# Optimization experiments

Measured on AMD Instinct MI355X. Metric: run time of the kernel, lower is better.

## Reference

```python
import jax, jax.numpy as jnp
import numpy as np

N_NODES = 50000
N_EDGES = 1600000
D_IN = 128
D_HID = 128
D_OUT = 3
EPS = 1e-5


def setup_inputs() -> dict:
    key = jax.random.key(0)
    ks = jax.random.split(key, 16)
    def lin(k, fi, fo):
        s = 1.0 / np.sqrt(fi)
        return jax.random.uniform(k, (fi, fo), jnp.float32, -s, s)
    inp = {
        "x": jax.random.normal(ks[0], (N_NODES, D_IN), jnp.float32),
        "edge_index": jax.random.randint(ks[1], (2, N_EDGES), 0, N_NODES, jnp.int32),
        "W1": lin(ks[2], D_IN, D_HID), "b1": jnp.zeros((D_HID,), jnp.float32),
        "W2": lin(ks[3], D_HID, D_HID), "b2": jnp.zeros((D_HID,), jnp.float32),
        "W3": lin(ks[4], D_HID, D_HID), "b3": jnp.zeros((D_HID,), jnp.float32),
        "g1": jnp.ones((D_HID,), jnp.float32), "beta1": jnp.zeros((D_HID,), jnp.float32),
        "g2": jnp.ones((D_HID,), jnp.float32), "beta2": jnp.zeros((D_HID,), jnp.float32),
        "Wp1": lin(ks[5], D_HID, D_HID), "bp1": jnp.zeros((D_HID,), jnp.float32),
        "Wp2": lin(ks[6], D_HID, D_OUT), "bp2": jnp.zeros((D_OUT,), jnp.float32),
    }
    return inp


def _gcn_norm(edge_index, n):
    # add self-loops, symmetric normalization (PyG GCNConv default)
    loops = jnp.arange(n, dtype=edge_index.dtype)
    row = jnp.concatenate([edge_index[0], loops])  # source
    col = jnp.concatenate([edge_index[1], loops])  # target
    deg = jax.ops.segment_sum(jnp.ones_like(col, jnp.float32), col, num_segments=n)
    dinv = jnp.where(deg > 0, jax.lax.rsqrt(deg), 0.0)
    norm = dinv[row] * dinv[col]  # [E+N]
    return row, col, norm


def _gcn_conv(x, W, b, row, col, norm, n):
    h = x @ W                                # [N, F]
    msg = h[row] * norm[:, None]             # [E+N, F] gather
    out = jax.ops.segment_sum(msg, col, num_segments=n)  # scatter-add
    return out + b


def _layernorm(x, g, beta):
    mu = jnp.mean(x, axis=-1, keepdims=True)
    var = jnp.var(x, axis=-1, keepdims=True)
    return (x - mu) * jax.lax.rsqrt(var + EPS) * g + beta


def reference(x, edge_index, W1, b1, W2, b2, W3, b3, g1, beta1, g2, beta2, Wp1, bp1, Wp2, bp2):
    n = x.shape[0]
    row, col, norm = _gcn_norm(edge_index, n)
    # layer 0
    h = _gcn_conv(x, W1, b1, row, col, norm, n)
    h = _layernorm(jax.nn.relu(h), g1, beta1)  # dropout = identity (eval mode)
    # layer 1
    h = _gcn_conv(h, W2, b2, row, col, norm, n)
    h = _layernorm(jax.nn.relu(h), g2, beta2)
    # layer 2 (no layernorm)
    h = _gcn_conv(h, W3, b3, row, col, norm, n)
    h = jax.nn.relu(h)
    # post-MP MLP head (dropout = identity in eval)
    h = h @ Wp1 + bp1
    return h @ Wp2 + bp2
```

## Files before the change

kernel.cpp:

```cpp
#include <hip/hip_runtime.h>
#include <hip/hip_bf16.h>

#define EPS_LN 1e-5f
#define NB    256
#define SEGCAP 16384

typedef int ivec4 __attribute__((ext_vector_type(4)));
typedef short bf16x8v __attribute__((ext_vector_type(8)));
typedef float f32x4v __attribute__((ext_vector_type(4)));
typedef unsigned short u16x8 __attribute__((ext_vector_type(8)));


__global__ __launch_bounds__(256) void bucket_hist(const int* __restrict__ col,
                                                   int* __restrict__ chunkBH,
                                                   int E, int per, int nbuck) {
    __shared__ int hist[256];
    int t = threadIdx.x;
    hist[t] = 0;
    __syncthreads();
    int s0 = blockIdx.x * per;
    int s1 = s0 + per; if (s1 > E) s1 = E;
    if (s0 < s1) {
        int q0 = s0 >> 2, q1 = s1 >> 2;
        for (int i = q0 + t; i < q1; i += 256) {
            ivec4 c = __builtin_nontemporal_load((const ivec4*)col + i);
            atomicAdd(&hist[c.x >> 8], 1);
            atomicAdd(&hist[c.y >> 8], 1);
            atomicAdd(&hist[c.z >> 8], 1);
            atomicAdd(&hist[c.w >> 8], 1);
        }
        for (int i = (q1 << 2) + t; i < s1; i += 256)
            atomicAdd(&hist[col[i] >> 8], 1);
    }
    __syncthreads();
    if (t < nbuck) chunkBH[blockIdx.x * 256 + t] = hist[t];
}

__global__ __launch_bounds__(256) void bucket_scan(int* __restrict__ chunkBH,
                                                   int* __restrict__ bucketStart,
                                                   int* __restrict__ rowPtr,
                                                   int E, int n, int nbuck, int nb) {
    __shared__ int tot[256];
    int t = threadIdx.x;
    int run = 0;
    if (t < nbuck) {
        for (int k0 = 0; k0 < nb; k0 += 16) {
            int v[16];
#pragma unroll
            for (int j = 0; j < 16; j++)
                v[j] = (k0 + j < nb) ? chunkBH[(k0 + j) * 256 + t] : 0;
#pragma unroll
            for (int j = 0; j < 16; j++) {
                int tv = v[j];
                if (k0 + j < nb) chunkBH[(k0 + j) * 256 + t] = run;
                run += tv;
            }
        }
    }
    tot[t] = run;
    __syncthreads();
    for (int d = 1; d < 256; d <<= 1) {
        int add = (t >= d) ? tot[t - d] : 0;
        __syncthreads();
        tot[t] += add;
        __syncthreads();
    }
    if (t < nbuck) bucketStart[t] = tot[t] - run;
    if (t == 0) { bucketStart[nbuck] = E; rowPtr[n] = E; }
}

__global__ __launch_bounds__(256) void scatter_pairs(const int* __restrict__ row,
                                                     const int* __restrict__ col,
                                                     const int* __restrict__ chunkBH,
                                                     const int* __restrict__ bucketStart,
                                                     unsigned long long* __restrict__ tmp,
                                                     int E, int per, int nbuck) {
    __shared__ int curs[256];
    int t = threadIdx.x;
    int k = blockIdx.x;
    curs[t] = (t < nbuck) ? (chunkBH[k * 256 + t] + bucketStart[t]) : 0;
    __syncthreads();
    int s0 = k * per;
    int s1 = s0 + per; if (s1 > E) s1 = E;
    if (s0 >= s1) return;
    int q0 = s0 >> 2, q1 = s1 >> 2;
    for (int i = q0 + t; i < q1; i += 256) {
        ivec4 c4 = __builtin_nontemporal_load((const ivec4*)col + i);
        ivec4 r4 = __builtin_nontemporal_load((const ivec4*)row + i);
        int p0 = atomicAdd(&curs[c4.x >> 8], 1);
        tmp[p0] = ((unsigned long long)(unsigned)c4.x << 32) | (unsigned)r4.x;
        int p1 = atomicAdd(&curs[c4.y >> 8], 1);
        tmp[p1] = ((unsigned long long)(unsigned)c4.y << 32) | (unsigned)r4.y;
        int p2 = atomicAdd(&curs[c4.z >> 8], 1);
        tmp[p2] = ((unsigned long long)(unsigned)c4.z << 32) | (unsigned)r4.z;
        int p3 = atomicAdd(&curs[c4.w >> 8], 1);
        tmp[p3] = ((unsigned long long)(unsigned)c4.w << 32) | (unsigned)r4.w;
    }
    for (int i = (q1 << 2) + t; i < s1; i += 256) {
        int c = col[i], r = row[i];
        int p = atomicAdd(&curs[c >> 8], 1);
        tmp[p] = ((unsigned long long)(unsigned)c << 32) | (unsigned)r;
    }
}

__global__ __launch_bounds__(256) void bucket_fill(const unsigned long long* __restrict__ tmp,
                                                   const int* __restrict__ bucketStart,
                                                   int* __restrict__ rowPtr,
                                                   float* __restrict__ dinv,
                                                   int* __restrict__ srcList,
                                                   int n) {
    __shared__ int cnt[256];
    __shared__ int cur[256];
    __shared__ int seg[SEGCAP];
    int b = blockIdx.x, t = threadIdx.x;
    int node0 = b << 8;
    int s0 = bucketStart[b], s1 = bucketStart[b + 1];
    int len = s1 - s0;
    cnt[t] = 0;
    __syncthreads();
    for (int i = s0 + t; i < s1; i += 256) {
        int c = (int)(tmp[i] >> 32);
        atomicAdd(&cnt[c - node0], 1);
    }
    __syncthreads();
    int v = cnt[t];
    cur[t] = v;
    __syncthreads();
    for (int d = 1; d < 256; d <<= 1) {
        int add = (t >= d) ? cur[t - d] : 0;
        __syncthreads();
        cur[t] += add;
        __syncthreads();
    }
    int excl = cur[t] - v;
    int node = node0 + t;
    if (node < n) {
        rowPtr[node] = s0 + excl;
        dinv[node] = rsqrtf((float)v + 1.0f);
    }
    cur[t] = excl;
    __syncthreads();
    if (len <= SEGCAP) {
        for (int i = s0 + t; i < s1; i += 256) {
            unsigned long long p = tmp[i];
            int c = (int)(p >> 32);
            int r = (int)(p & 0xffffffffu);
            int pos = atomicAdd(&cur[c - node0], 1);
            seg[pos] = r;
        }
        __syncthreads();
        for (int i = t; i < len; i += 256)
            srcList[s0 + i] = seg[i];
    } else {
        for (int i = s0 + t; i < s1; i += 256) {
            unsigned long long p = tmp[i];
            int c = (int)(p >> 32);
            int r = (int)(p & 0xffffffffu);
            int pos = atomicAdd(&cur[c - node0], 1);
            srcList[s0 + pos] = r;
        }
    }
}

__global__ __launch_bounds__(256) void pack_w_all(const float* __restrict__ W1,
                                                  const float* __restrict__ W2,
                                                  const float* __restrict__ W3,
                                                  unsigned short* __restrict__ Wq,
                                                  const float* __restrict__ Wp1,
                                                  const float* __restrict__ bp1,
                                                  const float* __restrict__ Wp2,
                                                  const float* __restrict__ bp2,
                                                  float* __restrict__ Weff,
                                                  float* __restrict__ beff) {
    if (blockIdx.x == 192) {
        __shared__ float w2[384];
        int t = threadIdx.x;
        for (int idx = t; idx < 384; idx += 256) w2[idx] = Wp2[idx];
        __syncthreads();
        if (t < 128) {
            float p0 = 0.f, p1 = 0.f, p2 = 0.f;
            const float* wr = Wp1 + (size_t)t * 128;
            for (int k = 0; k < 128; k++) {
                float v = wr[k];
                p0 += v * w2[k * 3 + 0];
                p1 += v * w2[k * 3 + 1];
                p2 += v * w2[k * 3 + 2];
            }
            Weff[t * 3 + 0] = p0; Weff[t * 3 + 1] = p1; Weff[t * 3 + 2] = p2;
            if (t == 0) {
                float q0 = bp2[0], q1 = bp2[1], q2 = bp2[2];
                for (int k = 0; k < 128; k++) {
                    float v = bp1[k];
                    q0 += v * w2[k * 3 + 0];
                    q1 += v * w2[k * 3 + 1];
                    q2 += v * w2[k * 3 + 2];
                }
                beff[0] = q0; beff[1] = q1; beff[2] = q2;
            }
        }
        return;
    }
    int w = blockIdx.x >> 6;
    const float* W = (w == 0) ? W1 : (w == 1) ? W2 : W3;
    unsigned short* Wp = Wq + (size_t)w * 32768;
    int s = (blockIdx.x & 63) * 256 + threadIdx.x;
    int i = s & 7;
    int lane = (s >> 3) & 63;
    int jt = (s >> 9) & 7;
    int kb = s >> 12;
    int k = kb * 32 + ((lane >> 4) & 3) * 8 + i;
    int nn = jt * 16 + (lane & 15);
    float v = W[k * 128 + nn];
    __hip_bfloat16 hi = __float2bfloat16(v);
    float hf = __bfloat162float(hi);
    __hip_bfloat16 lo = __float2bfloat16(v - hf);
    Wp[s]         = *(unsigned short*)&hi;
    Wp[16384 + s] = *(unsigned short*)&lo;
}

__device__ __forceinline__ void split8(const float* __restrict__ p,
                                       bf16x8v& ah, bf16x8v& al) {
#pragma unroll
    for (int i = 0; i < 8; i++) {
        float v = p[i];
        __hip_bfloat16 hb = __float2bfloat16(v);
        float hf = __bfloat162float(hb);
        __hip_bfloat16 lb = __float2bfloat16(v - hf);
        ah[i] = *(short*)&hb;
        al[i] = *(short*)&lb;
    }
}

template<int ASRC>
__global__ __launch_bounds__(256) void gemm_mfma(const float* __restrict__ Af32,
                                                 const unsigned short* __restrict__ Ahi,
                                                 const unsigned short* __restrict__ Alo,
                                                 const unsigned short* __restrict__ Wp,
                                                 const float* __restrict__ dinv,
                                                 unsigned short* __restrict__ hbOut,
                                                 int n) {
    __shared__ unsigned short Bs[8192];

    const int tx = threadIdx.x;
    const int wv = tx >> 6;
    const int l  = tx & 63;
    const int m0 = blockIdx.x * 64 + wv * 16;
    int arow = m0 + (l & 15);
    if (arow >= n) arow = 0;
    const int kofs = (l >> 4) * 8;

    f32x4v acc[8];
#pragma unroll
    for (int jt = 0; jt < 8; jt++) acc[jt] = (f32x4v){0.f, 0.f, 0.f, 0.f};

#pragma unroll
    for (int kb = 0; kb < 4; kb++) {
        __syncthreads();
        {
            u16x8* dH = (u16x8*)&Bs[tx * 16];
            const u16x8* sH = (const u16x8*)(Wp + kb * 4096 + tx * 16);
            dH[0] = sH[0]; dH[1] = sH[1];
            u16x8* dL = (u16x8*)&Bs[4096 + tx * 16];
            const u16x8* sL = (const u16x8*)(Wp + 16384 + kb * 4096 + tx * 16);
            dL[0] = sL[0]; dL[1] = sL[1];
        }
        bf16x8v ah, al;
        if (ASRC == 0) {
            split8(Af32 + (size_t)arow * 128 + kb * 32 + kofs, ah, al);
        } else {
            ah = *(const bf16x8v*)(Ahi + (size_t)arow * 128 + kb * 32 + kofs);
            al = *(const bf16x8v*)(Alo + (size_t)arow * 128 + kb * 32 + kofs);
        }
        __syncthreads();
#pragma unroll
        for (int jt = 0; jt < 8; jt++) {
            bf16x8v bh = *(const bf16x8v*)&Bs[jt * 512 + l * 8];
            bf16x8v bl = *(const bf16x8v*)&Bs[4096 + jt * 512 + l * 8];
            acc[jt] = __builtin_amdgcn_mfma_f32_16x16x32_bf16(ah, bh, acc[jt], 0, 0, 0);
            acc[jt] = __builtin_amdgcn_mfma_f32_16x16x32_bf16(ah, bl, acc[jt], 0, 0, 0);
            acc[jt] = __builtin_amdgcn_mfma_f32_16x16x32_bf16(al, bh, acc[jt], 0, 0, 0);
        }
    }

    const int r0 = m0 + (l >> 4) * 4;
    const int colb = l & 15;
#pragma unroll
    for (int r = 0; r < 4; r++) {
        int grow = r0 + r;
        if (grow < n) {
            float dv = dinv[grow];
#pragma unroll
            for (int jt = 0; jt < 8; jt++) {
                __hip_bfloat16 t = __float2bfloat16(acc[jt][r] * dv);
                hbOut[(size_t)grow * 128 + jt * 16 + colb] = *(unsigned short*)&t;
            }
        }
    }
}

#define BF_LO(u) __uint_as_float((u) << 16)
#define BF_HI(u) __uint_as_float((u) & 0xffff0000u)

#define ACC8(u)  do { \
    a[0] += BF_LO((u).x); a[1] += BF_HI((u).x); \
    a[2] += BF_LO((u).y); a[3] += BF_HI((u).y); \
    a[4] += BF_LO((u).z); a[5] += BF_HI((u).z); \
    a[6] += BF_LO((u).w); a[7] += BF_HI((u).w); } while (0)

__global__ __launch_bounds__(128) void agg_post(const unsigned int* __restrict__ hb,
                                                const int* __restrict__ rowPtr,
                                                const int* __restrict__ srcList,
                                                const float* __restrict__ dinv,
                                                const float* __restrict__ b,
                                                const float* __restrict__ g,
                                                const float* __restrict__ beta,
                                                unsigned short* __restrict__ outHi,
                                                unsigned short* __restrict__ outLo,
                                                int n) {
    int wid = (blockIdx.x * 128 + threadIdx.x) >> 6;
    int lane = threadIdx.x & 63;
    if (wid >= n) return;
    int h = lane & 15;
    int gg = lane >> 4;
    int e0 = rowPtr[wid], e1 = rowPtr[wid + 1];
    float dc = dinv[wid];
    const uint4* hb4 = (const uint4*)hb;

    uint4 us = hb4[(size_t)wid * 16 + h];

    float a[8];
#pragma unroll
    for (int j = 0; j < 8; j++) a[j] = 0.f;

    int idx0 = (e0 + 0 + gg < e1) ? srcList[e0 + 0 + gg] : -1;
    int idx1 = (e0 + 4 + gg < e1) ? srcList[e0 + 4 + gg] : -1;
    int idx2 = (e0 + 8 + gg < e1) ? srcList[e0 + 8 + gg] : -1;
    int idx3 = (e0 + 12 + gg < e1) ? srcList[e0 + 12 + gg] : -1;
    int e = e0;
    for (; e + 16 <= e1; e += 16) {
        int ni0 = (e + 16 + gg < e1) ? srcList[e + 16 + gg] : -1;
        int ni1 = (e + 20 + gg < e1) ? srcList[e + 20 + gg] : -1;
        int ni2 = (e + 24 + gg < e1) ? srcList[e + 24 + gg] : -1;
        int ni3 = (e + 28 + gg < e1) ? srcList[e + 28 + gg] : -1;
        uint4 u0 = hb4[(size_t)idx0 * 16 + h];
        uint4 u1 = hb4[(size_t)idx1 * 16 + h];
        uint4 u2 = hb4[(size_t)idx2 * 16 + h];
        uint4 u3 = hb4[(size_t)idx3 * 16 + h];
        ACC8(u0); ACC8(u1); ACC8(u2); ACC8(u3);
        idx0 = ni0; idx1 = ni1; idx2 = ni2; idx3 = ni3;
    }
    if (idx0 >= 0) { uint4 u = hb4[(size_t)idx0 * 16 + h]; ACC8(u); }
    if (idx1 >= 0) { uint4 u = hb4[(size_t)idx1 * 16 + h]; ACC8(u); }
    if (idx2 >= 0) { uint4 u = hb4[(size_t)idx2 * 16 + h]; ACC8(u); }
    if (idx3 >= 0) { uint4 u = hb4[(size_t)idx3 * 16 + h]; ACC8(u); }

#pragma unroll
    for (int j = 0; j < 8; j++) {
        a[j] += __shfl_xor(a[j], 16, 64);
        a[j] += __shfl_xor(a[j], 32, 64);
    }
    ACC8(us);

    float4 bv0 = *(const float4*)(b + h * 8);
    float4 bv1 = *(const float4*)(b + h * 8 + 4);
    a[0] = fmaxf(a[0] * dc + bv0.x, 0.f);
    a[1] = fmaxf(a[1] * dc + bv0.y, 0.f);
    a[2] = fmaxf(a[2] * dc + bv0.z, 0.f);
    a[3] = fmaxf(a[3] * dc + bv0.w, 0.f);
    a[4] = fmaxf(a[4] * dc + bv1.x, 0.f);
    a[5] = fmaxf(a[5] * dc + bv1.y, 0.f);
    a[6] = fmaxf(a[6] * dc + bv1.z, 0.f);
    a[7] = fmaxf(a[7] * dc + bv1.w, 0.f);

    float s = ((a[0] + a[1]) + (a[2] + a[3])) + ((a[4] + a[5]) + (a[6] + a[7]));
#pragma unroll
    for (int m = 8; m >= 1; m >>= 1) s += __shfl_xor(s, m, 64);
    float mu = s * (1.f / 128.f);
    float sq = 0.f;
    float d[8];
#pragma unroll
    for (int j = 0; j < 8; j++) { d[j] = a[j] - mu; sq += d[j] * d[j]; }
#pragma unroll
    for (int m = 8; m >= 1; m >>= 1) sq += __shfl_xor(sq, m, 64);
    float rs = rsqrtf(sq * (1.f / 128.f) + EPS_LN);
    float4 gv0 = *(const float4*)(g + h * 8);
    float4 gv1 = *(const float4*)(g + h * 8 + 4);
    float4 bt0 = *(const float4*)(beta + h * 8);
    float4 bt1 = *(const float4*)(beta + h * 8 + 4);
    a[0] = d[0] * rs * gv0.x + bt0.x;
    a[1] = d[1] * rs * gv0.y + bt0.y;
    a[2] = d[2] * rs * gv0.z + bt0.z;
    a[3] = d[3] * rs * gv0.w + bt0.w;
    a[4] = d[4] * rs * gv1.x + bt1.x;
    a[5] = d[5] * rs * gv1.y + bt1.y;
    a[6] = d[6] * rs * gv1.z + bt1.z;
    a[7] = d[7] * rs * gv1.w + bt1.w;

    if (gg == 0) {
        ushort4 h0, h1, l0, l1;
        __hip_bfloat16 bb; float ff;
        bb = __float2bfloat16(a[0]); ff = __bfloat162float(bb); h0.x = *(unsigned short*)&bb;
        bb = __float2bfloat16(a[0] - ff); l0.x = *(unsigned short*)&bb;
        bb = __float2bfloat16(a[1]); ff = __bfloat162float(bb); h0.y = *(unsigned short*)&bb;
        bb = __float2bfloat16(a[1] - ff); l0.y = *(unsigned short*)&bb;
        bb = __float2bfloat16(a[2]); ff = __bfloat162float(bb); h0.z = *(unsigned short*)&bb;
        bb = __float2bfloat16(a[2] - ff); l0.z = *(unsigned short*)&bb;
        bb = __float2bfloat16(a[3]); ff = __bfloat162float(bb); h0.w = *(unsigned short*)&bb;
        bb = __float2bfloat16(a[3] - ff); l0.w = *(unsigned short*)&bb;
        bb = __float2bfloat16(a[4]); ff = __bfloat162float(bb); h1.x = *(unsigned short*)&bb;
        bb = __float2bfloat16(a[4] - ff); l1.x = *(unsigned short*)&bb;
        bb = __float2bfloat16(a[5]); ff = __bfloat162float(bb); h1.y = *(unsigned short*)&bb;
        bb = __float2bfloat16(a[5] - ff); l1.y = *(unsigned short*)&bb;
        bb = __float2bfloat16(a[6]); ff = __bfloat162float(bb); h1.z = *(unsigned short*)&bb;
        bb = __float2bfloat16(a[6] - ff); l1.z = *(unsigned short*)&bb;
        bb = __float2bfloat16(a[7]); ff = __bfloat162float(bb); h1.w = *(unsigned short*)&bb;
        bb = __float2bfloat16(a[7] - ff); l1.w = *(unsigned short*)&bb;
        size_t base = (size_t)wid * 128 + h * 8;
        *(ushort4*)(outHi + base)     = h0;
        *(ushort4*)(outHi + base + 4) = h1;
        *(ushort4*)(outLo + base)     = l0;
        *(ushort4*)(outLo + base + 4) = l1;
    }
}

__global__ __launch_bounds__(128) void agg_head(
        const unsigned int* __restrict__ hb,
        const int* __restrict__ rowPtr,
        const int* __restrict__ srcList,
        const float* __restrict__ dinv,
        const float* __restrict__ b,
        const float* __restrict__ Weff,
        const float* __restrict__ beff,
        float* __restrict__ out, int n) {
    int tt = threadIdx.x;
    int wid = (blockIdx.x * 128 + tt) >> 6;
    int lane = tt & 63;
    if (wid >= n) return;
    int h = lane & 15;
    int gg = lane >> 4;
    int e0 = rowPtr[wid], e1 = rowPtr[wid + 1];
    float dc = dinv[wid];
    const uint4* hb4 = (const uint4*)hb;
    uint4 us = hb4[(size_t)wid * 16 + h];

    float wreg[24];
    {
        const float4* wp = (const float4*)(Weff + 24 * h);
#pragma unroll
        for (int q = 0; q < 6; q++) {
            float4 v = wp[q];
            wreg[4 * q + 0] = v.x; wreg[4 * q + 1] = v.y;
            wreg[4 * q + 2] = v.z; wreg[4 * q + 3] = v.w;
        }
    }

    float a[8];
#pragma unroll
    for (int j = 0; j < 8; j++) a[j] = 0.f;

    int idx0 = (e0 + 0 + gg < e1) ? srcList[e0 + 0 + gg] : -1;
    int idx1 = (e0 + 4 + gg < e1) ? srcList[e0 + 4 + gg] : -1;
    int idx2 = (e0 + 8 + gg < e1) ? srcList[e0 + 8 + gg] : -1;
    int idx3 = (e0 + 12 + gg < e1) ? srcList[e0 + 12 + gg] : -1;
    int e = e0;
    for (; e + 16 <= e1; e += 16) {
        int ni0 = (e + 16 + gg < e1) ? srcList[e + 16 + gg] : -1;
        int ni1 = (e + 20 + gg < e1) ? srcList[e + 20 + gg] : -1;
        int ni2 = (e + 24 + gg < e1) ? srcList[e + 24 + gg] : -1;
        int ni3 = (e + 28 + gg < e1) ? srcList[e + 28 + gg] : -1;
        uint4 u0 = hb4[(size_t)idx0 * 16 + h];
        uint4 u1 = hb4[(size_t)idx1 * 16 + h];
        uint4 u2 = hb4[(size_t)idx2 * 16 + h];
        uint4 u3 = hb4[(size_t)idx3 * 16 + h];
        ACC8(u0); ACC8(u1); ACC8(u2); ACC8(u3);
        idx0 = ni0; idx1 = ni1; idx2 = ni2; idx3 = ni3;
    }
    if (idx0 >= 0) { uint4 u = hb4[(size_t)idx0 * 16 + h]; ACC8(u); }
    if (idx1 >= 0) { uint4 u = hb4[(size_t)idx1 * 16 + h]; ACC8(u); }
    if (idx2 >= 0) { uint4 u = hb4[(size_t)idx2 * 16 + h]; ACC8(u); }
    if (idx3 >= 0) { uint4 u = hb4[(size_t)idx3 * 16 + h]; ACC8(u); }

#pragma unroll
    for (int j = 0; j < 8; j++) {
        a[j] += __shfl_xor(a[j], 16, 64);
        a[j] += __shfl_xor(a[j], 32, 64);
    }
    ACC8(us);

    float4 bv0 = *(const float4*)(b + h * 8);
    float4 bv1 = *(const float4*)(b + h * 8 + 4);
    a[0] = fmaxf(a[0] * dc + bv0.x, 0.f);
    a[1] = fmaxf(a[1] * dc + bv0.y, 0.f);
    a[2] = fmaxf(a[2] * dc + bv0.z, 0.f);
    a[3] = fmaxf(a[3] * dc + bv0.w, 0.f);
    a[4] = fmaxf(a[4] * dc + bv1.x, 0.f);
    a[5] = fmaxf(a[5] * dc + bv1.y, 0.f);
    a[6] = fmaxf(a[6] * dc + bv1.z, 0.f);
    a[7] = fmaxf(a[7] * dc + bv1.w, 0.f);

    float p0 = 0.f, p1 = 0.f, p2 = 0.f;
#pragma unroll
    for (int j = 0; j < 8; j++) {
        p0 += a[j] * wreg[j * 3 + 0];
        p1 += a[j] * wreg[j * 3 + 1];
        p2 += a[j] * wreg[j * 3 + 2];
    }
#pragma unroll
    for (int m = 8; m >= 1; m >>= 1) {
        p0 += __shfl_xor(p0, m, 64);
        p1 += __shfl_xor(p1, m, 64);
        p2 += __shfl_xor(p2, m, 64);
    }
    if (lane == 0) {
        out[(size_t)wid * 3 + 0] = p0 + beff[0];
        out[(size_t)wid * 3 + 1] = p1 + beff[1];
        out[(size_t)wid * 3 + 2] = p2 + beff[2];
    }
}

extern "C" void kernel_launch(void* const* d_in, const int* in_sizes, int n_in,
                              void* d_out, int out_size, void* d_ws, size_t ws_size,
                              hipStream_t stream) {
    const float* x   = (const float*)d_in[0];
    const int* ei    = (const int*)d_in[1];
    const float* W1  = (const float*)d_in[2];
    const float* b1  = (const float*)d_in[3];
    const float* W2  = (const float*)d_in[4];
    const float* b2  = (const float*)d_in[5];
    const float* W3  = (const float*)d_in[6];
    const float* b3  = (const float*)d_in[7];
    const float* g1  = (const float*)d_in[8];
    const float* be1 = (const float*)d_in[9];
    const float* g2  = (const float*)d_in[10];
    const float* be2 = (const float*)d_in[11];
    const float* Wp1f = (const float*)d_in[12];
    const float* bp1 = (const float*)d_in[13];
    const float* Wp2f = (const float*)d_in[14];
    const float* bp2 = (const float*)d_in[15];
    float* out = (float*)d_out;

    const int n = in_sizes[0] / 128;
    const int E = in_sizes[1] / 2;
    const int* row = ei;
    const int* col = ei + E;

    char* ws = (char*)d_ws;
    size_t nA  = ((size_t)n * 4 + 255) & ~(size_t)255;
    size_t nA1 = ((size_t)(n + 1) * 4 + 255) & ~(size_t)255;
    size_t eA  = ((size_t)E * 4 + 255) & ~(size_t)255;
    size_t hbSz = ((size_t)n * 128 * 2 + 255) & ~(size_t)255;
    int*   rowPtr  = (int*)ws;
    float* dinvp   = (float*)(ws + nA1);
    int*   srcList = (int*)(ws + nA1 + nA);
    unsigned short* hbA = (unsigned short*)(ws + nA1 + nA + eA);
    unsigned short* hbB = hbA + hbSz / 2;
    unsigned short* Phi = hbB + hbSz / 2;
    unsigned short* Plo = Phi + hbSz / 2;
    unsigned short* Wq  = Plo + hbSz / 2;
    float* Weff = (float*)(Wq + 3 * 32768);
    float* beff = Weff + 384;
    unsigned long long* tmp = (unsigned long long*)Phi;
    int* chunkBH     = (int*)((char*)Phi + 2 * eA);
    int* bucketStart = (int*)((char*)Phi + 2 * eA + (size_t)NB * 256 * 4);

    const int nbuck = (n + 255) >> 8;
    const int per   = (((E + NB - 1) / NB) + 15) & ~15;
    const int tileBlocks = (n + 63) / 64;
    const int nodeWaveBlocks = (n + 1) / 2;

    bucket_hist<<<NB, 256, 0, stream>>>(col, chunkBH, E, per, nbuck);
    bucket_scan<<<1, 256, 0, stream>>>(chunkBH, bucketStart, rowPtr, E, n, nbuck, NB);
    scatter_pairs<<<NB, 256, 0, stream>>>(row, col, chunkBH, bucketStart, tmp, E, per, nbuck);
    bucket_fill<<<nbuck, 256, 0, stream>>>(tmp, bucketStart, rowPtr, dinvp, srcList, n);
    pack_w_all<<<193, 256, 0, stream>>>(W1, W2, W3, Wq, Wp1f, bp1, Wp2f, bp2, Weff, beff);

    gemm_mfma<0><<<tileBlocks, 256, 0, stream>>>(x, nullptr, nullptr, Wq, dinvp, hbA, n);
    agg_post<<<nodeWaveBlocks, 128, 0, stream>>>((const unsigned int*)hbA,
                                                 rowPtr, srcList, dinvp,
                                                 b1, g1, be1, Phi, Plo, n);
    gemm_mfma<1><<<tileBlocks, 256, 0, stream>>>(nullptr, Phi, Plo, Wq + 32768, dinvp, hbB, n);
    agg_post<<<nodeWaveBlocks, 128, 0, stream>>>((const unsigned int*)hbB,
                                                 rowPtr, srcList, dinvp,
                                                 b2, g2, be2, Phi, Plo, n);
    gemm_mfma<1><<<tileBlocks, 256, 0, stream>>>(nullptr, Phi, Plo, Wq + 65536, dinvp, hbA, n);
    agg_head<<<nodeWaveBlocks, 128, 0, stream>>>((const unsigned int*)hbA,
                                                 rowPtr, srcList, dinvp,
                                                 b3, Weff, beff, out, n);
}
```

Before: 361.3 us.

## Use 512-thread GEMM blocks and shrink aggregation unroll to cut register use

The MFMA GEMM now runs 8 waves per block over 128 rows, so each weight tile staged in shared memory serves twice as many rows and each thread copies half as much of it. The aggregation kernels drop from four to two in-flight neighbour gathers per lane. The head kernel now loads the output-projection weights after aggregation instead of holding them in 24 registers throughout. The aim is lower register pressure and higher occupancy in the gather kernels, at the cost of fewer outstanding memory loads per wave.

```diff
diff --git a/kernel.cpp b/kernel.cpp
--- a/kernel.cpp
+++ b/kernel.cpp
@@ -232,7 +232,7 @@
 }
 
 template<int ASRC>
-__global__ __launch_bounds__(256) void gemm_mfma(const float* __restrict__ Af32,
+__global__ __launch_bounds__(512) void gemm_mfma(const float* __restrict__ Af32,
                                                  const unsigned short* __restrict__ Ahi,
                                                  const unsigned short* __restrict__ Alo,
                                                  const unsigned short* __restrict__ Wp,
@@ -244,7 +244,7 @@
     const int tx = threadIdx.x;
     const int wv = tx >> 6;
     const int l  = tx & 63;
-    const int m0 = blockIdx.x * 64 + wv * 16;
+    const int m0 = blockIdx.x * 128 + wv * 16;
     int arow = m0 + (l & 15);
     if (arow >= n) arow = 0;
     const int kofs = (l >> 4) * 8;
@@ -257,12 +257,8 @@
     for (int kb = 0; kb < 4; kb++) {
         __syncthreads();
         {
-            u16x8* dH = (u16x8*)&Bs[tx * 16];
-            const u16x8* sH = (const u16x8*)(Wp + kb * 4096 + tx * 16);
-            dH[0] = sH[0]; dH[1] = sH[1];
-            u16x8* dL = (u16x8*)&Bs[4096 + tx * 16];
-            const u16x8* sL = (const u16x8*)(Wp + 16384 + kb * 4096 + tx * 16);
-            dL[0] = sL[0]; dL[1] = sL[1];
+            *(u16x8*)&Bs[tx * 8]        = *(const u16x8*)(Wp + kb * 4096 + tx * 8);
+            *(u16x8*)&Bs[4096 + tx * 8] = *(const u16x8*)(Wp + 16384 + kb * 4096 + tx * 8);
         }
         bf16x8v ah, al;
         if (ASRC == 0) {
@@ -332,27 +328,19 @@
 #pragma unroll
     for (int j = 0; j < 8; j++) a[j] = 0.f;
 
-    int idx0 = (e0 + 0 + gg < e1) ? srcList[e0 + 0 + gg] : -1;
+    int idx0 = (e0 + gg < e1) ? srcList[e0 + gg] : -1;
     int idx1 = (e0 + 4 + gg < e1) ? srcList[e0 + 4 + gg] : -1;
-    int idx2 = (e0 + 8 + gg < e1) ? srcList[e0 + 8 + gg] : -1;
-    int idx3 = (e0 + 12 + gg < e1) ? srcList[e0 + 12 + gg] : -1;
     int e = e0;
-    for (; e + 16 <= e1; e += 16) {
-        int ni0 = (e + 16 + gg < e1) ? srcList[e + 16 + gg] : -1;
-        int ni1 = (e + 20 + gg < e1) ? srcList[e + 20 + gg] : -1;
-        int ni2 = (e + 24 + gg < e1) ? srcList[e + 24 + gg] : -1;
-        int ni3 = (e + 28 + gg < e1) ? srcList[e + 28 + gg] : -1;
+    for (; e + 8 <= e1; e += 8) {
+        int ni0 = (e + 8 + gg < e1) ? srcList[e + 8 + gg] : -1;
+        int ni1 = (e + 12 + gg < e1) ? srcList[e + 12 + gg] : -1;
         uint4 u0 = hb4[(size_t)idx0 * 16 + h];
         uint4 u1 = hb4[(size_t)idx1 * 16 + h];
-        uint4 u2 = hb4[(size_t)idx2 * 16 + h];
-        uint4 u3 = hb4[(size_t)idx3 * 16 + h];
-        ACC8(u0); ACC8(u1); ACC8(u2); ACC8(u3);
-        idx0 = ni0; idx1 = ni1; idx2 = ni2; idx3 = ni3;
+        ACC8(u0); ACC8(u1);
+        idx0 = ni0; idx1 = ni1;
     }
     if (idx0 >= 0) { uint4 u = hb4[(size_t)idx0 * 16 + h]; ACC8(u); }
     if (idx1 >= 0) { uint4 u = hb4[(size_t)idx1 * 16 + h]; ACC8(u); }
-    if (idx2 >= 0) { uint4 u = hb4[(size_t)idx2 * 16 + h]; ACC8(u); }
-    if (idx3 >= 0) { uint4 u = hb4[(size_t)idx3 * 16 + h]; ACC8(u); }
 
 #pragma unroll
     for (int j = 0; j < 8; j++) {
@@ -443,42 +431,23 @@
     const uint4* hb4 = (const uint4*)hb;
     uint4 us = hb4[(size_t)wid * 16 + h];
 
-    float wreg[24];
-    {
-        const float4* wp = (const float4*)(Weff + 24 * h);
-#pragma unroll
-        for (int q = 0; q < 6; q++) {
-            float4 v = wp[q];
-            wreg[4 * q + 0] = v.x; wreg[4 * q + 1] = v.y;
-            wreg[4 * q + 2] = v.z; wreg[4 * q + 3] = v.w;
-        }
-    }
-
     float a[8];
 #pragma unroll
     for (int j = 0; j < 8; j++) a[j] = 0.f;
 
-    int idx0 = (e0 + 0 + gg < e1) ? srcList[e0 + 0 + gg] : -1;
+    int idx0 = (e0 + gg < e1) ? srcList[e0 + gg] : -1;
     int idx1 = (e0 + 4 + gg < e1) ? srcList[e0 + 4 + gg] : -1;
-    int idx2 = (e0 + 8 + gg < e1) ? srcList[e0 + 8 + gg] : -1;
-    int idx3 = (e0 + 12 + gg < e1) ? srcList[e0 + 12 + gg] : -1;
     int e = e0;
-    for (; e + 16 <= e1; e += 16) {
-        int ni0 = (e + 16 + gg < e1) ? srcList[e + 16 + gg] : -1;
-        int ni1 = (e + 20 + gg < e1) ? srcList[e + 20 + gg] : -1;
-        int ni2 = (e + 24 + gg < e1) ? srcList[e + 24 + gg] : -1;
-        int ni3 = (e + 28 + gg < e1) ? srcList[e + 28 + gg] : -1;
+    for (; e + 8 <= e1; e += 8) {
+        int ni0 = (e + 8 + gg < e1) ? srcList[e + 8 + gg] : -1;
+        int ni1 = (e + 12 + gg < e1) ? srcList[e + 12 + gg] : -1;
         uint4 u0 = hb4[(size_t)idx0 * 16 + h];
         uint4 u1 = hb4[(size_t)idx1 * 16 + h];
-        uint4 u2 = hb4[(size_t)idx2 * 16 + h];
-        uint4 u3 = hb4[(size_t)idx3 * 16 + h];
-        ACC8(u0); ACC8(u1); ACC8(u2); ACC8(u3);
-        idx0 = ni0; idx1 = ni1; idx2 = ni2; idx3 = ni3;
+        ACC8(u0); ACC8(u1);
+        idx0 = ni0; idx1 = ni1;
     }
     if (idx0 >= 0) { uint4 u = hb4[(size_t)idx0 * 16 + h]; ACC8(u); }
     if (idx1 >= 0) { uint4 u = hb4[(size_t)idx1 * 16 + h]; ACC8(u); }
-    if (idx2 >= 0) { uint4 u = hb4[(size_t)idx2 * 16 + h]; ACC8(u); }
-    if (idx3 >= 0) { uint4 u = hb4[(size_t)idx3 * 16 + h]; ACC8(u); }
 
 #pragma unroll
     for (int j = 0; j < 8; j++) {
@@ -499,11 +468,18 @@
     a[7] = fmaxf(a[7] * dc + bv1.w, 0.f);
 
     float p0 = 0.f, p1 = 0.f, p2 = 0.f;
-#pragma unroll
-    for (int j = 0; j < 8; j++) {
-        p0 += a[j] * wreg[j * 3 + 0];
-        p1 += a[j] * wreg[j * 3 + 1];
-        p2 += a[j] * wreg[j * 3 + 2];
+    {
+        const float4* wp = (const float4*)(Weff + 24 * h);
+#pragma unroll
+        for (int q = 0; q < 2; q++) {
+            float4 w0 = wp[3 * q + 0];
+            float4 w1 = wp[3 * q + 1];
+            float4 w2 = wp[3 * q + 2];
+            const float* aw = &a[4 * q];
+            p0 += aw[0] * w0.x + aw[1] * w0.w + aw[2] * w1.z + aw[3] * w2.y;
+            p1 += aw[0] * w0.y + aw[1] * w1.x + aw[2] * w1.w + aw[3] * w2.z;
+            p2 += aw[0] * w0.z + aw[1] * w1.y + aw[2] * w2.x + aw[3] * w2.w;
+        }
     }
 #pragma unroll
     for (int m = 8; m >= 1; m >>= 1) {
@@ -565,7 +541,7 @@
 
     const int nbuck = (n + 255) >> 8;
     const int per   = (((E + NB - 1) / NB) + 15) & ~15;
-    const int tileBlocks = (n + 63) / 64;
+    const int tileBlocks = (n + 127) / 128;
     const int nodeWaveBlocks = (n + 1) / 2;
 
     bucket_hist<<<NB, 256, 0, stream>>>(col, chunkBH, E, per, nbuck);
@@ -574,15 +550,15 @@
     bucket_fill<<<nbuck, 256, 0, stream>>>(tmp, bucketStart, rowPtr, dinvp, srcList, n);
     pack_w_all<<<193, 256, 0, stream>>>(W1, W2, W3, Wq, Wp1f, bp1, Wp2f, bp2, Weff, beff);
 
-    gemm_mfma<0><<<tileBlocks, 256, 0, stream>>>(x, nullptr, nullptr, Wq, dinvp, hbA, n);
+    gemm_mfma<0><<<tileBlocks, 512, 0, stream>>>(x, nullptr, nullptr, Wq, dinvp, hbA, n);
     agg_post<<<nodeWaveBlocks, 128, 0, stream>>>((const unsigned int*)hbA,
                                                  rowPtr, srcList, dinvp,
                                                  b1, g1, be1, Phi, Plo, n);
-    gemm_mfma<1><<<tileBlocks, 256, 0, stream>>>(nullptr, Phi, Plo, Wq + 32768, dinvp, hbB, n);
+    gemm_mfma<1><<<tileBlocks, 512, 0, stream>>>(nullptr, Phi, Plo, Wq + 32768, dinvp, hbB, n);
     agg_post<<<nodeWaveBlocks, 128, 0, stream>>>((const unsigned int*)hbB,
                                                  rowPtr, srcList, dinvp,
                                                  b2, g2, be2, Phi, Plo, n);
-    gemm_mfma<1><<<tileBlocks, 256, 0, stream>>>(nullptr, Phi, Plo, Wq + 65536, dinvp, hbA, n);
+    gemm_mfma<1><<<tileBlocks, 512, 0, stream>>>(nullptr, Phi, Plo, Wq + 65536, dinvp, hbA, n);
     agg_head<<<nodeWaveBlocks, 128, 0, stream>>>((const unsigned int*)hbA,
                                                  rowPtr, srcList, dinvp,
                                                  b3, Weff, beff, out, n);
```

Result: no change. 356.5 us (-1.3%).
